# Optimization experiments

Measured on AMD Instinct MI355X. Metric: run time of the kernel, lower is better.

## Reference

```python
import jax, jax.numpy as jnp
import numpy as np

EPS = 1e-5

def setup_inputs() -> dict:
    key = jax.random.key(0)
    k1, k2 = jax.random.split(key)
    x = jax.random.normal(k1, (32, 256, 56, 56), dtype=jnp.float32)
    # Conv2d(in=2, out=1, k=7, bias=False) weight: [out, in, kh, kw]
    conv_w = jax.random.normal(k2, (1, 2, 7, 7), dtype=jnp.float32) * 0.1
    # BatchNorm2d(1) params/buffers (eval mode)
    gamma = jnp.ones((1,), dtype=jnp.float32)
    beta = jnp.zeros((1,), dtype=jnp.float32)
    running_mean = jnp.zeros((1,), dtype=jnp.float32)
    running_var = jnp.ones((1,), dtype=jnp.float32)
    return {"x": x, "conv_w": conv_w, "gamma": gamma, "beta": beta,
            "running_mean": running_mean, "running_var": running_var}

def reference(x, conv_w, gamma, beta, running_mean, running_var):
    # channel-wise max & mean -> [B,2,H,W]
    max_result = jnp.max(x, axis=1, keepdims=True)
    avg_result = jnp.mean(x, axis=1, keepdims=True)
    result = jnp.concatenate([max_result, avg_result], axis=1)
    # 7x7 conv, pad=3, NCHW / OIHW
    out = jax.lax.conv_general_dilated(
        result, conv_w, window_strides=(1, 1), padding=((3, 3), (3, 3)),
        dimension_numbers=("NCHW", "OIHW", "NCHW"))
    # BatchNorm2d(1), eval mode with running stats
    inv = gamma / jnp.sqrt(running_var + EPS)
    out = (out - running_mean[None, :, None, None]) * inv[None, :, None, None] + beta[None, :, None, None]
    gate = jax.nn.sigmoid(out)  # [B,1,H,W]
    return x * gate
```

## Files before the change

### kernel.cpp

```cpp
#include <hip/hip_runtime.h>
#include <math.h>

#define NB 32
#define NC 256
#define SH 56
#define SW 56
#define HW 3136
#define HW4 784

__global__ __launch_bounds__(256) void k_reduce(const float4* __restrict__ x,
                                                float4* __restrict__ mx_out,
                                                float4* __restrict__ av_out) {
    __shared__ float4 smax[8][32];
    __shared__ float4 ssum[8][32];
    const int tid = threadIdx.x;
    const int pos = tid & 31;
    const int cg  = tid >> 5;
    const unsigned g = blockIdx.x * 32u + pos;
    const int b  = (int)(g / HW4);
    const int p4 = (int)(g - (unsigned)b * HW4);
    const float4* base = x + ((size_t)b * NC) * HW4 + p4 + (size_t)(cg * 32) * HW4;

    const float NEG = -__builtin_inff();
    float4 vmax = make_float4(NEG, NEG, NEG, NEG);
    float4 vsum = make_float4(0.f, 0.f, 0.f, 0.f);
    #pragma unroll 8
    for (int c = 0; c < 32; ++c) {
        float4 v = base[(size_t)c * HW4];
        vmax.x = fmaxf(vmax.x, v.x); vmax.y = fmaxf(vmax.y, v.y);
        vmax.z = fmaxf(vmax.z, v.z); vmax.w = fmaxf(vmax.w, v.w);
        vsum.x += v.x; vsum.y += v.y; vsum.z += v.z; vsum.w += v.w;
    }
    smax[cg][pos] = vmax;
    ssum[cg][pos] = vsum;
    __syncthreads();
    if (tid < 32) {
        float4 m = smax[0][tid];
        float4 s = ssum[0][tid];
        #pragma unroll
        for (int q = 1; q < 8; ++q) {
            float4 mm = smax[q][tid];
            float4 ss = ssum[q][tid];
            m.x = fmaxf(m.x, mm.x); m.y = fmaxf(m.y, mm.y);
            m.z = fmaxf(m.z, mm.z); m.w = fmaxf(m.w, mm.w);
            s.x += ss.x; s.y += ss.y; s.z += ss.z; s.w += ss.w;
        }
        const float r = 1.0f / 256.0f;
        s.x *= r; s.y *= r; s.z *= r; s.w *= r;
        const unsigned go = blockIdx.x * 32u + tid;
        mx_out[go] = m;
        av_out[go] = s;
    }
}

__global__ __launch_bounds__(256) void k_conv(const float* __restrict__ mx,
                                              const float* __restrict__ av,
                                              const float* __restrict__ cw,
                                              const float* __restrict__ gamma,
                                              const float* __restrict__ beta,
                                              const float* __restrict__ rmean,
                                              const float* __restrict__ rvar,
                                              float* __restrict__ gate) {
    __shared__ float swm[49];
    __shared__ float swa[49];
    __shared__ float sbias;
    const int tid = threadIdx.x;
    const float inv = gamma[0] * rsqrtf(rvar[0] + 1e-5f);
    if (tid < 49)                swm[tid]      = cw[tid]      * inv;
    else if (tid < 98)           swa[tid - 49] = cw[tid]      * inv;
    if (tid == 0)                sbias = beta[0] - rmean[0] * inv;
    __syncthreads();

    const int idx = blockIdx.x * 256 + tid;
    const int b = idx / HW;
    const int p = idx - b * HW;
    const int h = p / SW;
    const int w = p - h * SW;
    const float* mrow = mx + (size_t)b * HW;
    const float* arow = av + (size_t)b * HW;

    float acc = sbias;
    #pragma unroll
    for (int kh = 0; kh < 7; ++kh) {
        const int hh = h + kh - 3;
        if (hh < 0 || hh >= SH) continue;
        #pragma unroll
        for (int kw = 0; kw < 7; ++kw) {
            const int ww = w + kw - 3;
            if (ww < 0 || ww >= SW) continue;
            const int q = hh * SW + ww;
            acc += mrow[q] * swm[kh * 7 + kw] + arow[q] * swa[kh * 7 + kw];
        }
    }
    gate[idx] = 1.0f / (1.0f + expf(-acc));
}

__global__ __launch_bounds__(256) void k_mul(const float4* __restrict__ x,
                                             const float4* __restrict__ gate,
                                             float4* __restrict__ out) {
    const unsigned total = (unsigned)NB * NC * HW4;
    const unsigned stride = gridDim.x * 256u;
    for (unsigned v = blockIdx.x * 256u + threadIdx.x; v < total; v += stride) {
        const unsigned row = v / HW4;
        const unsigned p4  = v - row * HW4;
        const unsigned b   = row >> 8;
        const float4 g4 = gate[b * HW4 + p4];
        const float4 xv = x[v];
        out[v] = make_float4(xv.x * g4.x, xv.y * g4.y, xv.z * g4.z, xv.w * g4.w);
    }
}

extern "C" void kernel_launch(void* const* d_in, const int* in_sizes, int n_in,
                              void* d_out, int out_size, void* d_ws, size_t ws_size,
                              hipStream_t stream) {
    const float* x     = (const float*)d_in[0];
    const float* cw    = (const float*)d_in[1];
    const float* gamma = (const float*)d_in[2];
    const float* beta  = (const float*)d_in[3];
    const float* rmean = (const float*)d_in[4];
    const float* rvar  = (const float*)d_in[5];
    float* out = (float*)d_out;

    float* mx_p   = (float*)d_ws;
    float* av_p   = mx_p + (size_t)NB * HW;
    float* gate_p = av_p + (size_t)NB * HW;

    k_reduce<<<(NB * HW4) / 32, 256, 0, stream>>>(
        (const float4*)x, (float4*)mx_p, (float4*)av_p);

    k_conv<<<(NB * HW) / 256, 256, 0, stream>>>(
        mx_p, av_p, cw, gamma, beta, rmean, rvar, gate_p);

    k_mul<<<2048, 256, 0, stream>>>(
        (const float4*)x, (const float4*)gate_p, (float4*)out);
}
```

Baseline: 65.34 us.

## Fuse conv gate computation into the broadcast multiply kernel per two-row strip

Merges the 7x7 conv/sigmoid kernel and the gating multiply into a single kernel. Each block computes the gate for two image rows of one batch into shared memory, then multiplies those rows across all 256 channels. This drops one launch and the gate round-trip through global memory. In exchange, each block reads 28-float4 strided segments per channel, which may coalesce less well than the flat streaming multiply, and the grid shrinks to 896 blocks.

```diff
diff --git a/kernel.cpp b/kernel.cpp
--- a/kernel.cpp
+++ b/kernel.cpp
@@ -53,60 +53,62 @@
     }
 }
 
-__global__ __launch_bounds__(256) void k_conv(const float* __restrict__ mx,
-                                              const float* __restrict__ av,
-                                              const float* __restrict__ cw,
-                                              const float* __restrict__ gamma,
-                                              const float* __restrict__ beta,
-                                              const float* __restrict__ rmean,
-                                              const float* __restrict__ rvar,
-                                              float* __restrict__ gate) {
-    __shared__ float swm[49];
-    __shared__ float swa[49];
+__global__ __launch_bounds__(256) void k_conv_mul(const float* __restrict__ mx,
+                                                  const float* __restrict__ av,
+                                                  const float* __restrict__ cw,
+                                                  const float* __restrict__ gamma,
+                                                  const float* __restrict__ beta,
+                                                  const float* __restrict__ rmean,
+                                                  const float* __restrict__ rvar,
+                                                  const float4* __restrict__ x,
+                                                  float4* __restrict__ out) {
+    __shared__ float sw[98];
     __shared__ float sbias;
+    __shared__ float4 sgate4[28];
+
     const int tid = threadIdx.x;
+    const int b  = blockIdx.x / 28;
+    const int rp = blockIdx.x - b * 28;
+
     const float inv = gamma[0] * rsqrtf(rvar[0] + 1e-5f);
-    if (tid < 49)                swm[tid]      = cw[tid]      * inv;
-    else if (tid < 98)           swa[tid - 49] = cw[tid]      * inv;
-    if (tid == 0)                sbias = beta[0] - rmean[0] * inv;
+    if (tid < 98) sw[tid] = cw[tid] * inv;
+    if (tid == 0) sbias = beta[0] - rmean[0] * inv;
     __syncthreads();
 
-    const int idx = blockIdx.x * 256 + tid;
-    const int b = idx / HW;
-    const int p = idx - b * HW;
-    const int h = p / SW;
-    const int w = p - h * SW;
-    const float* mrow = mx + (size_t)b * HW;
-    const float* arow = av + (size_t)b * HW;
+    if (tid < 112) {
+        const int h = rp * 2 + (tid / 56 ? 1 : 0) + 0 * tid;
+        const int hr = rp * 2 + (tid >= 56 ? 1 : 0);
+        const int w  = tid - (tid >= 56 ? 56 : 0);
+        const float* mrow = mx + (size_t)b * HW;
+        const float* arow = av + (size_t)b * HW;
+        float acc = sbias;
+        #pragma unroll
+        for (int kh = 0; kh < 7; ++kh) {
+            const int hh = hr + kh - 3;
+            if (hh < 0 || hh >= SH) continue;
+            #pragma unroll
+            for (int kw = 0; kw < 7; ++kw) {
+                const int ww = w + kw - 3;
+                if (ww < 0 || ww >= SW) continue;
+                const int q = hh * SW + ww;
+                acc += mrow[q] * sw[kh * 7 + kw] + arow[q] * sw[49 + kh * 7 + kw];
+            }
+        }
+        ((float*)sgate4)[tid] = 1.0f / (1.0f + expf(-acc));
+        (void)h;
+    }
+    __syncthreads();
 
-    float acc = sbias;
-    #pragma unroll
-    for (int kh = 0; kh < 7; ++kh) {
-        const int hh = h + kh - 3;
-        if (hh < 0 || hh >= SH) continue;
-        #pragma unroll
-        for (int kw = 0; kw < 7; ++kw) {
-            const int ww = w + kw - 3;
-            if (ww < 0 || ww >= SW) continue;
-            const int q = hh * SW + ww;
-            acc += mrow[q] * swm[kh * 7 + kw] + arow[q] * swa[kh * 7 + kw];
-        }
-    }
-    gate[idx] = 1.0f / (1.0f + expf(-acc));
-}
-
-__global__ __launch_bounds__(256) void k_mul(const float4* __restrict__ x,
-                                             const float4* __restrict__ gate,
-                                             float4* __restrict__ out) {
-    const unsigned total = (unsigned)NB * NC * HW4;
-    const unsigned stride = gridDim.x * 256u;
-    for (unsigned v = blockIdx.x * 256u + threadIdx.x; v < total; v += stride) {
-        const unsigned row = v / HW4;
-        const unsigned p4  = v - row * HW4;
-        const unsigned b   = row >> 8;
-        const float4 g4 = gate[b * HW4 + p4];
-        const float4 xv = x[v];
-        out[v] = make_float4(xv.x * g4.x, xv.y * g4.y, xv.z * g4.z, xv.w * g4.w);
+    const size_t strip = (size_t)b * NC * HW4 + (size_t)rp * 28;
+    #pragma unroll 4
+    for (int it = 0; it < 28; ++it) {
+        const unsigned idx = (unsigned)it * 256u + (unsigned)tid;
+        const unsigned c = idx / 28u;
+        const unsigned q = idx - c * 28u;
+        const size_t off = strip + (size_t)c * HW4 + q;
+        const float4 g  = sgate4[q];
+        const float4 xv = x[off];
+        out[off] = make_float4(xv.x * g.x, xv.y * g.y, xv.z * g.z, xv.w * g.w);
     }
 }
 
@@ -121,16 +123,13 @@
     const float* rvar  = (const float*)d_in[5];
     float* out = (float*)d_out;
 
-    float* mx_p   = (float*)d_ws;
-    float* av_p   = mx_p + (size_t)NB * HW;
-    float* gate_p = av_p + (size_t)NB * HW;
+    float* mx_p = (float*)d_ws;
+    float* av_p = mx_p + (size_t)NB * HW;
 
     k_reduce<<<(NB * HW4) / 32, 256, 0, stream>>>(
         (const float4*)x, (float4*)mx_p, (float4*)av_p);
 
-    k_conv<<<(NB * HW) / 256, 256, 0, stream>>>(
-        mx_p, av_p, cw, gamma, beta, rmean, rvar, gate_p);
-
-    k_mul<<<2048, 256, 0, stream>>>(
-        (const float4*)x, (const float4*)gate_p, (float4*)out);
+    k_conv_mul<<<NB * 28, 256, 0, stream>>>(
+        mx_p, av_p, cw, gamma, beta, rmean, rvar,
+        (const float4*)x, (float4*)out);
 }
```

Result: faster. 63.10 us (-3.4%).
